# Optimization experiments

Measured on AMD Instinct MI355X. Metric: run time of the kernel, lower is better.

## Reference

```python
import jax, jax.numpy as jnp
import numpy as np
import math

L, N, D = 1024, 64, 64
O = 1024

def setup_inputs() -> dict:
    key = jax.random.key(0)
    k1, k2 = jax.random.split(key)
    x = jax.random.normal(k1, (L, N, D), dtype=jnp.float32)
    upfold = jax.random.normal(k2, (O, N, D), dtype=jnp.float32)
    return {"x": x, "upfold": upfold}

def reference(x, upfold):
    # x: [L, N, D], upfold: [O, N, D]
    d = x.shape[-1]
    scale = 1.0 / math.sqrt(d)
    # affinities: [L, O, N]
    affinities = jnp.einsum('lnd,ond->lon', x, upfold) * scale
    # weighted sum with (sigmoid - 0.5) weights: [L, N, D]
    features = jnp.einsum('lon,ond->lnd', jax.nn.sigmoid(affinities) - 0.5, upfold)
    return features
```

## Files before the change

### kernel.cpp

```cpp
#include <hip/hip_runtime.h>
#include <stdint.h>

#define L_DIM 1024
#define N_DIM 64
#define D_DIM 64
#define O_DIM 1024
#define ND    4096
#define UPAD  72
#define NT    8

typedef float    floatx16 __attribute__((ext_vector_type(16)));
typedef _Float16 half8    __attribute__((ext_vector_type(8)));
typedef _Float16 h2       __attribute__((ext_vector_type(2)));
typedef __fp16   fp16x2   __attribute__((ext_vector_type(2)));

__device__ __forceinline__ uint32_t pkh2(float a, float b) {
    fp16x2 p = __builtin_amdgcn_cvt_pkrtz(a, b);
    return __builtin_bit_cast(uint32_t, p);
}

__device__ __forceinline__ half8 mk_frag(uint32_t a, uint32_t b, uint32_t c, uint32_t d) {
    union { uint32_t u[4]; half8 v; } U;
    U.u[0] = a; U.u[1] = b; U.u[2] = c; U.u[3] = d;
    return U.v;
}

__device__ __forceinline__ uint32_t psig(float s0, float s1) {
    const h2 HI = {(_Float16)41.6f,        (_Float16)41.6f};
    const h2 LO = {(_Float16)-41.6f,       (_Float16)-41.6f};
    const h2 SC = {(_Float16)0.0625f,      (_Float16)0.0625f};
    const h2 C0 = {(_Float16)0.03099238f,  (_Float16)0.03099238f};
    const h2 C1 = {(_Float16)-0.00842090f, (_Float16)-0.00842090f};
    const h2 C2 = {(_Float16)0.00151845f,  (_Float16)0.00151845f};
    const h2 C3 = {(_Float16)-1.02197e-4f, (_Float16)-1.02197e-4f};
    h2 s = __builtin_bit_cast(h2, pkh2(s0, s1));
    s = __builtin_elementwise_min(s, HI);
    s = __builtin_elementwise_max(s, LO);
    h2 ha = s * SC;
    h2 v  = ha * ha;
    h2 w  = C2 + v * C3;
    w     = C1 + v * w;
    w     = C0 + v * w;
    h2 f  = s * w;
    return __builtin_bit_cast(uint32_t, f);
}

__device__ __forceinline__ void load_tile(const float* ubase, int team, int ot,
                                          int rp, int cq, float* va, float* vb) {
    const float* pr = ubase + (size_t)(team * 512 + ot * 64 + 2 * rp) * ND + 16 * cq;
    #pragma unroll
    for (int j = 0; j < 4; ++j) {
        float4 f = *(const float4*)(pr + 4 * j);
        va[4*j] = f.x; va[4*j+1] = f.y; va[4*j+2] = f.z; va[4*j+3] = f.w;
        float4 g = *(const float4*)(pr + ND + 4 * j);
        vb[4*j] = g.x; vb[4*j+1] = g.y; vb[4*j+2] = g.z; vb[4*j+3] = g.w;
    }
}

__global__ void __launch_bounds__(256, 4)
corr_kernel(const float* __restrict__ x, const float* __restrict__ up,
            float* __restrict__ out)
{
    __shared__ __align__(16) unsigned char smem[36864];
    uint16_t (*Ub)[64][UPAD] = (uint16_t (*)[64][UPAD])smem;
    uint16_t (*Ut)[64][UPAD] = (uint16_t (*)[64][UPAD])(smem + 18432);
    float    (*Fred)[2][2][32][16] = (float (*)[2][2][32][16])smem;
    float    (*Xs)[68] = (float (*)[68])smem;

    const int tid  = threadIdx.x;
    const int lane = tid & 63;
    const int wid  = tid >> 6;
    const int l31  = lane & 31;
    const int h    = lane >> 5;
    const int team = wid >> 1;
    const int wrow = wid & 1;
    const int ttid = tid & 127;
    const int rp   = ttid & 31;
    const int cq   = ttid >> 5;
    const int n    = blockIdx.x;
    const int lb   = blockIdx.y;
    const int lw   = lb * 64 + wrow * 32 + l31;

    const float* ubase = up + (size_t)n * D_DIM;

    float va[16], vb[16];
    load_tile(ubase, team, 0, rp, cq, va, vb);

    half8 Xf[4];
    {
        const int xr = tid >> 2;
        const int xc = tid & 3;
        const float* xsrc = x + (size_t)(lb * 64 + xr) * ND + n * D_DIM;
        #pragma unroll
        for (int j = 0; j < 4; ++j) {
            float4 f = *(const float4*)(xsrc + 4 * (xc + 4 * j));
            *(float4*)&Xs[xr][4 * (xc + 4 * j)] = f;
        }
        __syncthreads();
        const int rl = wrow * 32 + l31;
        #pragma unroll
        for (int kk = 0; kk < 4; ++kk) {
            float4 f1 = *(const float4*)&Xs[rl][16 * kk + 8 * h];
            float4 f2 = *(const float4*)&Xs[rl][16 * kk + 8 * h + 4];
            Xf[kk] = mk_frag(pkh2(f1.x, f1.y), pkh2(f1.z, f1.w),
                             pkh2(f2.x, f2.y), pkh2(f2.z, f2.w));
        }
        __syncthreads();
    }

    floatx16 F0, F1;
    #pragma unroll
    for (int i = 0; i < 16; ++i) { F0[i] = 0.0f; F1[i] = 0.0f; }

    for (int ot = 0; ot < NT; ++ot) {
        *(uint4*)&Ub[team][2*rp][16*cq] =
            make_uint4(pkh2(va[0],va[1]),  pkh2(va[2],va[3]),
                       pkh2(va[4],va[5]),  pkh2(va[6],va[7]));
        *(uint4*)&Ub[team][2*rp][16*cq + 8] =
            make_uint4(pkh2(va[8],va[9]),  pkh2(va[10],va[11]),
                       pkh2(va[12],va[13]),pkh2(va[14],va[15]));
        *(uint4*)&Ub[team][2*rp+1][16*cq] =
            make_uint4(pkh2(vb[0],vb[1]),  pkh2(vb[2],vb[3]),
                       pkh2(vb[4],vb[5]),  pkh2(vb[6],vb[7]));
        *(uint4*)&Ub[team][2*rp+1][16*cq + 8] =
            make_uint4(pkh2(vb[8],vb[9]),  pkh2(vb[10],vb[11]),
                       pkh2(vb[12],vb[13]),pkh2(vb[14],vb[15]));
        #pragma unroll
        for (int j = 0; j < 16; ++j)
            *(uint32_t*)&Ut[team][16*cq + j][2*rp] = pkh2(va[j], vb[j]);
        __syncthreads();

        if (ot + 1 < NT)
            load_tile(ubase, team, ot + 1, rp, cq, va, vb);

        floatx16 S0, S1;
        #pragma unroll
        for (int i = 0; i < 16; ++i) { S0[i] = 0.0f; S1[i] = 0.0f; }
        #pragma unroll
        for (int kk = 0; kk < 4; ++kk) {
            half8 A0 = *(const half8*)&Ub[team][l31][16 * kk + 8 * h];
            half8 A1 = *(const half8*)&Ub[team][32 + l31][16 * kk + 8 * h];
            S0 = __builtin_amdgcn_mfma_f32_32x32x16_f16(A0, Xf[kk], S0, 0, 0, 0);
            S1 = __builtin_amdgcn_mfma_f32_32x32x16_f16(A1, Xf[kk], S1, 0, 0, 0);
        }

        uint32_t P[16];
        #pragma unroll
        for (int m = 0; m < 8; ++m) P[m]     = psig(S0[2*m], S0[2*m+1]);
        #pragma unroll
        for (int m = 0; m < 8; ++m) P[8 + m] = psig(S1[2*m], S1[2*m+1]);

        uint32_t R[8];
        #pragma unroll
        for (int c = 0; c < 4; ++c) {
            const uint32_t* Q = P + (c >> 1) * 8;
            const int t4 = (c & 1) * 4;
            R[2*c]   = __shfl_xor(h ? Q[t4]     : Q[t4 + 2], 32);
            R[2*c+1] = __shfl_xor(h ? Q[t4 + 1] : Q[t4 + 3], 32);
        }
        #pragma unroll
        for (int c = 0; c < 4; ++c) {
            const uint32_t* Q = P + (c >> 1) * 8;
            const int t4 = (c & 1) * 4;
            half8 B = h ? mk_frag(R[2*c], R[2*c+1], Q[t4 + 2], Q[t4 + 3])
                        : mk_frag(Q[t4], Q[t4 + 1], R[2*c], R[2*c+1]);
            half8 A0 = *(const half8*)&Ut[team][l31][16 * c + 8 * h];
            half8 A1 = *(const half8*)&Ut[team][32 + l31][16 * c + 8 * h];
            F0 = __builtin_amdgcn_mfma_f32_32x32x16_f16(A0, B, F0, 0, 0, 0);
            F1 = __builtin_amdgcn_mfma_f32_32x32x16_f16(A1, B, F1, 0, 0, 0);
        }
        __syncthreads();
    }

    {
        float* dst = &Fred[team][wrow][h][l31][0];
        const floatx16& Fexp = team ? F0 : F1;
        #pragma unroll
        for (int q = 0; q < 4; ++q)
            *(float4*)(dst + 4*q) = make_float4(Fexp[4*q], Fexp[4*q+1], Fexp[4*q+2], Fexp[4*q+3]);
    }
    __syncthreads();

    float* op = out + (size_t)lw * ND + n * D_DIM;
    if (team == 0) {
        const float* src = &Fred[1][wrow][h][l31][0];
        #pragma unroll
        for (int q = 0; q < 4; ++q) {
            float4 r = *(const float4*)(src + 4*q);
            float4 a; a.x = F0[4*q]   + r.x; a.y = F0[4*q+1] + r.y;
                      a.z = F0[4*q+2] + r.z; a.w = F0[4*q+3] + r.w;
            *(float4*)(op + 8*q + 4*h) = a;
        }
    } else {
        const float* src = &Fred[0][wrow][h][l31][0];
        #pragma unroll
        for (int q = 0; q < 4; ++q) {
            float4 r = *(const float4*)(src + 4*q);
            float4 a; a.x = F1[4*q]   + r.x; a.y = F1[4*q+1] + r.y;
                      a.z = F1[4*q+2] + r.z; a.w = F1[4*q+3] + r.w;
            *(float4*)(op + 32 + 8*q + 4*h) = a;
        }
    }
}

extern "C" void kernel_launch(void* const* d_in, const int* in_sizes, int n_in,
                              void* d_out, int out_size, void* d_ws, size_t ws_size,
                              hipStream_t stream)
{
    const float* x  = (const float*)d_in[0];
    const float* up = (const float*)d_in[1];
    float* out      = (float*)d_out;
    dim3 grid(N_DIM, L_DIM / 64);
    corr_kernel<<<grid, dim3(256), 0, stream>>>(x, up, out);
}
```

Measured before the change: 109.5 us.

## Restructure upfold tile staging to vector-wide LDS stores with pair-packed transpose

```diff
diff --git a/kernel.cpp b/kernel.cpp
--- a/kernel.cpp
+++ b/kernel.cpp
@@ -6,7 +6,6 @@
 #define D_DIM 64
 #define O_DIM 1024
 #define ND    4096
-#define UPAD  72
 #define NT    8
 
 typedef float    floatx16 __attribute__((ext_vector_type(16)));
@@ -46,14 +45,12 @@
 }
 
 __device__ __forceinline__ void load_tile(const float* ubase, int team, int ot,
-                                          int rp, int cq, float* va, float* vb) {
-    const float* pr = ubase + (size_t)(team * 512 + ot * 64 + 2 * rp) * ND + 16 * cq;
+                                          int g, int c, float4* va, float4* vb) {
+    const float* pr = ubase + (size_t)(team * 512 + ot * 64 + 2 * g) * ND + 4 * c;
     #pragma unroll
     for (int j = 0; j < 4; ++j) {
-        float4 f = *(const float4*)(pr + 4 * j);
-        va[4*j] = f.x; va[4*j+1] = f.y; va[4*j+2] = f.z; va[4*j+3] = f.w;
-        float4 g = *(const float4*)(pr + ND + 4 * j);
-        vb[4*j] = g.x; vb[4*j+1] = g.y; vb[4*j+2] = g.z; vb[4*j+3] = g.w;
+        va[j] = *(const float4*)(pr + (size_t)(16 * j) * ND);
+        vb[j] = *(const float4*)(pr + (size_t)(16 * j) * ND + ND);
     }
 }
 
@@ -62,8 +59,8 @@
             float* __restrict__ out)
 {
     __shared__ __align__(16) unsigned char smem[36864];
-    uint16_t (*Ub)[64][UPAD] = (uint16_t (*)[64][UPAD])smem;
-    uint16_t (*Ut)[64][UPAD] = (uint16_t (*)[64][UPAD])(smem + 18432);
+    uint16_t (*Ub)[64][72]  = (uint16_t (*)[64][72])smem;
+    uint32_t (*Ut2)[32][68] = (uint32_t (*)[32][68])(smem + 18432);
     float    (*Fred)[2][2][32][16] = (float (*)[2][2][32][16])smem;
     float    (*Xs)[68] = (float (*)[68])smem;
 
@@ -75,16 +72,16 @@
     const int team = wid >> 1;
     const int wrow = wid & 1;
     const int ttid = tid & 127;
-    const int rp   = ttid & 31;
-    const int cq   = ttid >> 5;
+    const int c    = ttid & 15;
+    const int g    = ttid >> 4;
     const int n    = blockIdx.x;
     const int lb   = blockIdx.y;
     const int lw   = lb * 64 + wrow * 32 + l31;
 
     const float* ubase = up + (size_t)n * D_DIM;
 
-    float va[16], vb[16];
-    load_tile(ubase, team, 0, rp, cq, va, vb);
+    float4 va[4], vb[4];
+    load_tile(ubase, team, 0, g, c, va, vb);
 
     half8 Xf[4];
     {
@@ -113,25 +110,20 @@
     for (int i = 0; i < 16; ++i) { F0[i] = 0.0f; F1[i] = 0.0f; }
 
     for (int ot = 0; ot < NT; ++ot) {
-        *(uint4*)&Ub[team][2*rp][16*cq] =
-            make_uint4(pkh2(va[0],va[1]),  pkh2(va[2],va[3]),
-                       pkh2(va[4],va[5]),  pkh2(va[6],va[7]));
-        *(uint4*)&Ub[team][2*rp][16*cq + 8] =
-            make_uint4(pkh2(va[8],va[9]),  pkh2(va[10],va[11]),
-                       pkh2(va[12],va[13]),pkh2(va[14],va[15]));
-        *(uint4*)&Ub[team][2*rp+1][16*cq] =
-            make_uint4(pkh2(vb[0],vb[1]),  pkh2(vb[2],vb[3]),
-                       pkh2(vb[4],vb[5]),  pkh2(vb[6],vb[7]));
-        *(uint4*)&Ub[team][2*rp+1][16*cq + 8] =
-            make_uint4(pkh2(vb[8],vb[9]),  pkh2(vb[10],vb[11]),
-                       pkh2(vb[12],vb[13]),pkh2(vb[14],vb[15]));
-        #pragma unroll
-        for (int j = 0; j < 16; ++j)
-            *(uint32_t*)&Ut[team][16*cq + j][2*rp] = pkh2(va[j], vb[j]);
+        #pragma unroll
+        for (int j = 0; j < 4; ++j) {
+            uint2 ea = make_uint2(pkh2(va[j].x, va[j].y), pkh2(va[j].z, va[j].w));
+            uint2 eb = make_uint2(pkh2(vb[j].x, vb[j].y), pkh2(vb[j].z, vb[j].w));
+            *(uint2*)&Ub[team][2*g + 16*j][4*c]     = ea;
+            *(uint2*)&Ub[team][2*g + 16*j + 1][4*c] = eb;
+            uint4 et = make_uint4(pkh2(va[j].x, vb[j].x), pkh2(va[j].y, vb[j].y),
+                                  pkh2(va[j].z, vb[j].z), pkh2(va[j].w, vb[j].w));
+            *(uint4*)&Ut2[team][g + 8*j][4*c] = et;
+        }
         __syncthreads();
 
         if (ot + 1 < NT)
-            load_tile(ubase, team, ot + 1, rp, cq, va, vb);
+            load_tile(ubase, team, ot + 1, g, c, va, vb);
 
         floatx16 S0, S1;
         #pragma unroll
@@ -152,20 +144,28 @@
 
         uint32_t R[8];
         #pragma unroll
-        for (int c = 0; c < 4; ++c) {
-            const uint32_t* Q = P + (c >> 1) * 8;
-            const int t4 = (c & 1) * 4;
-            R[2*c]   = __shfl_xor(h ? Q[t4]     : Q[t4 + 2], 32);
-            R[2*c+1] = __shfl_xor(h ? Q[t4 + 1] : Q[t4 + 3], 32);
-        }
-        #pragma unroll
-        for (int c = 0; c < 4; ++c) {
-            const uint32_t* Q = P + (c >> 1) * 8;
-            const int t4 = (c & 1) * 4;
-            half8 B = h ? mk_frag(R[2*c], R[2*c+1], Q[t4 + 2], Q[t4 + 3])
-                        : mk_frag(Q[t4], Q[t4 + 1], R[2*c], R[2*c+1]);
-            half8 A0 = *(const half8*)&Ut[team][l31][16 * c + 8 * h];
-            half8 A1 = *(const half8*)&Ut[team][32 + l31][16 * c + 8 * h];
+        for (int c2 = 0; c2 < 4; ++c2) {
+            const uint32_t* Q = P + (c2 >> 1) * 8;
+            const int t4 = (c2 & 1) * 4;
+            R[2*c2]   = __shfl_xor(h ? Q[t4]     : Q[t4 + 2], 32);
+            R[2*c2+1] = __shfl_xor(h ? Q[t4 + 1] : Q[t4 + 3], 32);
+        }
+        #pragma unroll
+        for (int c2 = 0; c2 < 4; ++c2) {
+            const uint32_t* Q = P + (c2 >> 1) * 8;
+            const int t4 = (c2 & 1) * 4;
+            half8 B = h ? mk_frag(R[2*c2], R[2*c2+1], Q[t4 + 2], Q[t4 + 3])
+                        : mk_frag(Q[t4], Q[t4 + 1], R[2*c2], R[2*c2+1]);
+            const int opb = 8 * c2 + 4 * h;
+            const uint32_t* utp = &Ut2[team][0][0];
+            uint32_t a0[4], a1[4];
+            #pragma unroll
+            for (int k = 0; k < 4; ++k) {
+                a0[k] = utp[(opb + k) * 68 + l31];
+                a1[k] = utp[(opb + k) * 68 + 32 + l31];
+            }
+            half8 A0 = mk_frag(a0[0], a0[1], a0[2], a0[3]);
+            half8 A1 = mk_frag(a1[0], a1[1], a1[2], a1[3]);
             F0 = __builtin_amdgcn_mfma_f32_32x32x16_f16(A0, B, F0, 0, 0, 0);
             F1 = __builtin_amdgcn_mfma_f32_32x32x16_f16(A1, B, F1, 0, 0, 0);
         }
```

Measured after the change: 104.1 us. 4.9% less time.
